# Optimization experiments

Hardware: AMD Instinct MI355X
Metric: run time of the kernel (lower is better)

## Reference

```python
import jax, jax.numpy as jnp
import numpy as np

N_QUBITS = 10
N_GEN = 4
Q_DEPTH = 6
BATCH = 1024


def _cz_chain_diag(n):
    # Diagonal of the CZ chain CZ(0,1) CZ(1,2) ... CZ(n-2,n-1):
    # phase (-1)^(# adjacent 1-1 pairs) per computational basis state.
    idx = np.arange(2 ** n)
    bits = (idx[:, None] >> np.arange(n - 1, -1, -1)) & 1  # wire 0 = most significant (PennyLane)
    pairs = (bits[:, :-1] & bits[:, 1:]).sum(axis=1)
    return ((-1.0) ** pairs).astype(np.float32).reshape((2,) * n)

_CZ = jnp.asarray(_cz_chain_diag(N_QUBITS))


def _ry(t):
    c = jnp.cos(0.5 * t)
    s = jnp.sin(0.5 * t)
    return jnp.stack([jnp.stack([c, -s]), jnp.stack([s, c])]).astype(jnp.complex64)


def _rx(t):
    c = jnp.cos(0.5 * t).astype(jnp.complex64)
    js = (1j * jnp.sin(0.5 * t)).astype(jnp.complex64)
    return jnp.stack([jnp.stack([c, -js]), jnp.stack([-js, c])])


def _apply_1q(state, gate, wire):
    # state: (2,)*n complex statevector; apply 2x2 gate on `wire`.
    state = jnp.moveaxis(state, wire, -1)
    state = jnp.einsum('...j,ij->...i', state, gate)
    return jnp.moveaxis(state, -1, wire)


def _circuit(noise_s, weights, cz):
    # noise_s: (n_qubits,), weights: (q_depth, n_qubits)
    n = noise_s.shape[0]
    state = jnp.zeros((2,) * n, jnp.complex64).at[(0,) * n].set(1.0)
    for q in range(n):
        state = _apply_1q(state, _ry(noise_s[q]), q)
        state = _apply_1q(state, _rx(noise_s[q]), q)

    def layer(st, w):
        for q in range(n):
            st = _apply_1q(st, _ry(w[q]), q)
        return st * cz, None

    state, _ = jax.lax.scan(layer, state, weights)
    # <X_q> = Re <psi| X_q |psi>; X_q flips the q-th wire.
    return jnp.stack([jnp.real(jnp.vdot(state, jnp.flip(state, axis=q))) for q in range(n)])


def setup_inputs() -> dict:
    key = jax.random.key(0)
    k1, k2 = jax.random.split(key)
    noise = jax.random.normal(k1, (BATCH, N_QUBITS), dtype=jnp.float32)
    q_params = jax.random.uniform(k2, (N_GEN, Q_DEPTH, N_QUBITS), dtype=jnp.float32)  # q_delta=1.0 * rand
    return {"noise": noise, "q_params": q_params}


def reference(noise, q_params):
    per_sample = lambda ns, w: _circuit(ns, w, _CZ)
    per_gen = jax.vmap(lambda w: jax.vmap(lambda ns: per_sample(ns, w))(noise))(q_params)  # (G, B, n)
    out = jnp.transpose(per_gen, (1, 0, 2)).reshape(noise.shape[0], N_GEN * N_QUBITS)
    return out.astype(jnp.float32)
```

## Files before the change

### kernel.cpp

```cpp
#include <hip/hip_runtime.h>

#define NQ 10
#define NG 4
#define QD 6
#define NBATCH 1024
#define WPB 4


typedef unsigned u2v __attribute__((ext_vector_type(2)));

template<int CTRL, int RM, int BM, bool BC>
__device__ __forceinline__ float dppmov(float x) {
    return __int_as_float(__builtin_amdgcn_update_dpp(
        0, __float_as_int(x), CTRL, RM, BM, BC));
}
template<int CTRL>
__device__ __forceinline__ float dpp1(float x) { return dppmov<CTRL,0xF,0xF,true>(x); }

struct FX1 { static __device__ __forceinline__ float f(float x){ return dpp1<0xB1>(x); } };
struct FX2 { static __device__ __forceinline__ float f(float x){ return dpp1<0x4E>(x); } };
struct FX4 { static __device__ __forceinline__ float f(float x){ return dpp1<0x1B>(dpp1<0x141>(x)); } };
struct FX8 { static __device__ __forceinline__ float f(float x){ return dpp1<0x128>(x); } };
struct FX16 {
    static __device__ __forceinline__ float f(float x){
        return __int_as_float(__builtin_amdgcn_ds_swizzle(__float_as_int(x), 0x401F));
    }
};
struct FX32 {
    static __device__ __forceinline__ float f(float x){ return __shfl_xor(x, 32, 64); }
};

__device__ __forceinline__ float rlane(float v, int idx) {
    return __int_as_float(__builtin_amdgcn_readlane(__float_as_int(v), idx));
}

#if __has_builtin(__builtin_amdgcn_permlane32_swap) && __has_builtin(__builtin_amdgcn_permlane16_swap)
#define HAVE_SWAP 1
__device__ __forceinline__ void plswap32(float &a, float &b) {
    u2v r = __builtin_amdgcn_permlane32_swap(__float_as_uint(a), __float_as_uint(b), false, false);
    a = __uint_as_float(r.x); b = __uint_as_float(r.y);
}
__device__ __forceinline__ void plswap16(float &a, float &b) {
    u2v r = __builtin_amdgcn_permlane16_swap(__float_as_uint(a), __float_as_uint(b), false, false);
    a = __uint_as_float(r.x); b = __uint_as_float(r.y);
}
__device__ __forceinline__ void tr_b5b3(float (&s)[16]) {
#pragma unroll
    for (int j = 0; j < 8; ++j) plswap32(s[j], s[j + 8]);
}
__device__ __forceinline__ void tr_b4b2(float (&s)[16]) {
#pragma unroll
    for (int jj = 0; jj < 8; ++jj) {
        const int j = (jj & 3) | ((jj >> 2) << 3);
        plswap16(s[j], s[j + 4]);
    }
}
#else
#define HAVE_SWAP 0
#endif

__device__ __forceinline__ float wave_reduce(float x) {
    x += dppmov<0x111,0xF,0xF,true >(x);
    x += dppmov<0x112,0xF,0xF,true >(x);
    x += dppmov<0x114,0xF,0xF,true >(x);
    x += dppmov<0x118,0xF,0xF,true >(x);
    x += dppmov<0x142,0xA,0xF,false>(x);
    x += dppmov<0x143,0xC,0xF,false>(x);
    return __int_as_float(__builtin_amdgcn_readlane(__float_as_int(x), 63));
}

template<int M>
__device__ __forceinline__ void intra_rot1(float (&s)[16], float c, float sn) {
#pragma unroll
    for (int j = 0; j < 16; ++j)
        if ((j & M) == 0) {
            const int k = j | M;
            float v0 = s[j], v1 = s[k];
            s[j] = c * v0 - sn * v1;
            s[k] = sn * v0 + c * v1;
        }
}

template<class PF, int LM>
__device__ __forceinline__ void cross_rot(float (&sr)[16], float (&si)[16],
                                          float c, float sn, int lane) {
    const float sv = (lane & LM) ? sn : -sn;
#pragma unroll
    for (int j = 0; j < 16; ++j) {
        float pr = PF::f(sr[j]);
        sr[j] = c * sr[j] + sv * pr;
        float pi = PF::f(si[j]);
        si[j] = c * si[j] + sv * pi;
    }
}

template<class PF>
__device__ __forceinline__ float cross_exp(const float (&sr)[16], const float (&si)[16]) {
    float a = 0.f;
#pragma unroll
    for (int j = 0; j < 16; ++j) {
        a += sr[j] * PF::f(sr[j]);
        a += si[j] * PF::f(si[j]);
    }
    return a;
}

template<int M>
__device__ __forceinline__ float intra_exp(const float (&sr)[16], const float (&si)[16]) {
    float a = 0.f;
#pragma unroll
    for (int j = 0; j < 16; ++j)
        a += sr[j] * sr[j ^ M] + si[j] * si[j ^ M];
    return a;
}

__global__ __launch_bounds__(64 * WPB) void qsim_kernel(
    const float* __restrict__ noise,
    const float* __restrict__ qp,
    float* __restrict__ out)
{
    const int wave = threadIdx.x >> 6;
    const int lane = threadIdx.x & 63;
    const int g    = blockIdx.x & 3;
    const int b    = (blockIdx.x >> 2) * WPB + wave;

    float wcv, wsv;
    {
        const int widx = (lane < QD * NQ) ? lane : 0;
        __sincosf(0.5f * qp[g * (QD * NQ) + widx], &wsv, &wcv);
    }

    float sr[16], si[16];
    {
        float nc[NQ], ns[NQ];
#pragma unroll
        for (int q = 0; q < NQ; ++q)
            __sincosf(0.5f * noise[b * NQ + q], &ns[q], &nc[q]);

        auto facr = [&](int q, int bit) { return bit ? nc[q]*ns[q] : nc[q]*nc[q]; };
        auto faci = [&](int q, int bit) { return bit ? -nc[q]*ns[q] : -ns[q]*ns[q]; };

        float hr = 1.f, hi = 0.f;
#pragma unroll
        for (int p = 4; p <= 9; ++p) {
            const int q = NQ - 1 - p, bit = (lane >> (p - 4)) & 1;
            float fr = facr(q, bit), fi = faci(q, bit);
            float tr = hr * fr - hi * fi;
            float ti = hr * fi + hi * fr;
            hr = tr; hi = ti;
        }
        float t01r[4], t01i[4], t23r[4], t23i[4];
#pragma unroll
        for (int a = 0; a < 4; ++a) {
            float f9r = facr(9, a & 1), f9i = faci(9, a & 1);
            float f8r = facr(8, (a >> 1) & 1), f8i = faci(8, (a >> 1) & 1);
            t01r[a] = f9r * f8r - f9i * f8i;
            t01i[a] = f9r * f8i + f9i * f8r;
            float f7r = facr(7, a & 1), f7i = faci(7, a & 1);
            float f6r = facr(6, (a >> 1) & 1), f6i = faci(6, (a >> 1) & 1);
            t23r[a] = f7r * f6r - f7i * f6i;
            t23i[a] = f7r * f6i + f7i * f6r;
        }
        float prer[4], prei[4];
#pragma unroll
        for (int a = 0; a < 4; ++a) {
            prer[a] = hr * t01r[a] - hi * t01i[a];
            prei[a] = hr * t01i[a] + hi * t01r[a];
        }
#pragma unroll
        for (int j = 0; j < 16; ++j) {
            sr[j] = prer[j & 3] * t23r[j >> 2] - prei[j & 3] * t23i[j >> 2];
            si[j] = prer[j & 3] * t23i[j >> 2] + prei[j & 3] * t23r[j >> 2];
        }
    }

    unsigned czm[16];
#pragma unroll
    for (int j = 0; j < 16; ++j) {
        unsigned i = ((unsigned)lane << 4) | (unsigned)j;
        czm[j] = (unsigned)(__popc(i & (i >> 1)) & 1) << 31;
    }

#pragma unroll 1
    for (int l = 0; l < QD; ++l) {
        const int base = l * NQ;
        float c[NQ], sn[NQ];
#pragma unroll
        for (int q = 0; q < NQ; ++q) {
            c[q]  = rlane(wcv, base + q);
            sn[q] = rlane(wsv, base + q);
        }

        intra_rot1<1>(sr, c[9], sn[9]); intra_rot1<1>(si, c[9], sn[9]);
        intra_rot1<2>(sr, c[8], sn[8]); intra_rot1<2>(si, c[8], sn[8]);
        intra_rot1<4>(sr, c[7], sn[7]); intra_rot1<4>(si, c[7], sn[7]);
        intra_rot1<8>(sr, c[6], sn[6]); intra_rot1<8>(si, c[6], sn[6]);
        cross_rot<FX1, 1>(sr, si, c[5], sn[5], lane);
        cross_rot<FX2, 2>(sr, si, c[4], sn[4], lane);
        cross_rot<FX4, 4>(sr, si, c[3], sn[3], lane);
        cross_rot<FX8, 8>(sr, si, c[2], sn[2], lane);
#if HAVE_SWAP
        tr_b5b3(sr); tr_b5b3(si);
        tr_b4b2(sr); tr_b4b2(si);
        intra_rot1<8>(sr, c[0], sn[0]); intra_rot1<8>(si, c[0], sn[0]);
        intra_rot1<4>(sr, c[1], sn[1]); intra_rot1<4>(si, c[1], sn[1]);
        tr_b4b2(sr); tr_b4b2(si);
        tr_b5b3(sr); tr_b5b3(si);
#else
        cross_rot<FX32,32>(sr, si, c[0], sn[0], lane);
        cross_rot<FX16,16>(sr, si, c[1], sn[1], lane);
#endif
#pragma unroll
        for (int j = 0; j < 16; ++j) {
            sr[j] = __uint_as_float(__float_as_uint(sr[j]) ^ czm[j]);
            si[j] = __uint_as_float(__float_as_uint(si[j]) ^ czm[j]);
        }
    }

    float outval = 0.f;
    {
        float e9 = wave_reduce(intra_exp<1>(sr, si));
        float e8 = wave_reduce(intra_exp<2>(sr, si));
        float e7 = wave_reduce(intra_exp<4>(sr, si));
        float e6 = wave_reduce(intra_exp<8>(sr, si));
        float e5 = wave_reduce(cross_exp<FX1>(sr, si));
        float e4 = wave_reduce(cross_exp<FX2>(sr, si));
        float e3 = wave_reduce(cross_exp<FX4>(sr, si));
        float e2 = wave_reduce(cross_exp<FX8>(sr, si));
        float e0, e1;
#if HAVE_SWAP
        tr_b5b3(sr); tr_b5b3(si);
        tr_b4b2(sr); tr_b4b2(si);
        e0 = wave_reduce(intra_exp<8>(sr, si));
        e1 = wave_reduce(intra_exp<4>(sr, si));
#else
        e0 = wave_reduce(cross_exp<FX32>(sr, si));
        e1 = wave_reduce(cross_exp<FX16>(sr, si));
#endif
        outval = (lane == 0) ? e0 : outval;
        outval = (lane == 1) ? e1 : outval;
        outval = (lane == 2) ? e2 : outval;
        outval = (lane == 3) ? e3 : outval;
        outval = (lane == 4) ? e4 : outval;
        outval = (lane == 5) ? e5 : outval;
        outval = (lane == 6) ? e6 : outval;
        outval = (lane == 7) ? e7 : outval;
        outval = (lane == 8) ? e8 : outval;
        outval = (lane == 9) ? e9 : outval;
    }

    if (lane < NQ)
        out[b * (NG * NQ) + g * NQ + lane] = outval;
}

extern "C" void kernel_launch(void* const* d_in, const int* in_sizes, int n_in,
                              void* d_out, int out_size, void* d_ws, size_t ws_size,
                              hipStream_t stream) {
    const float* noise = (const float*)d_in[0];
    const float* qp    = (const float*)d_in[1];
    float* out = (float*)d_out;

    const int nblocks = (NBATCH * NG) / WPB;
    qsim_kernel<<<nblocks, 64 * WPB, 0, stream>>>(noise, qp, out);
}
```

Before: 99.51 us.

## Factor cosines out of RY rotations and apply combined scale at output

Each RY rotation is rewritten as [1,-t;t,1] with t=tan(theta/2). This turns every pair update into a single FMA, and the product of all cosines (squared) is applied once to the final expectation values. The CZ sign masks are now derived from four per-lane constants instead of a 16-entry array, which lowers register use, and the launch bounds now ask for 2 blocks per CU. This removes multiplies and half the readlanes per layer, but tan can blow up for angles near pi, and there is a numerical risk if cos is near zero.

```diff
diff --git a/kernel.cpp b/kernel.cpp
--- a/kernel.cpp
+++ b/kernel.cpp
@@ -69,28 +69,36 @@
     return __int_as_float(__builtin_amdgcn_readlane(__float_as_int(x), 63));
 }
 
+__device__ __forceinline__ float wave_product(float x) {
+    x *= dpp1<0xB1>(x);
+    x *= dpp1<0x4E>(x);
+    x *= dpp1<0x1B>(dpp1<0x141>(x));
+    x *= dpp1<0x128>(x);
+    x *= FX16::f(x);
+    x *= FX32::f(x);
+    return x;
+}
+
 template<int M>
-__device__ __forceinline__ void intra_rot1(float (&s)[16], float c, float sn) {
+__device__ __forceinline__ void intra_rot_t(float (&s)[16], float t) {
 #pragma unroll
     for (int j = 0; j < 16; ++j)
         if ((j & M) == 0) {
             const int k = j | M;
             float v0 = s[j], v1 = s[k];
-            s[j] = c * v0 - sn * v1;
-            s[k] = sn * v0 + c * v1;
+            s[j] = fmaf(-t, v1, v0);
+            s[k] = fmaf( t, v0, v1);
         }
 }
 
 template<class PF, int LM>
-__device__ __forceinline__ void cross_rot(float (&sr)[16], float (&si)[16],
-                                          float c, float sn, int lane) {
-    const float sv = (lane & LM) ? sn : -sn;
+__device__ __forceinline__ void cross_rot_t(float (&sr)[16], float (&si)[16],
+                                            float t, int lane) {
+    const float sv = (lane & LM) ? t : -t;
 #pragma unroll
     for (int j = 0; j < 16; ++j) {
-        float pr = PF::f(sr[j]);
-        sr[j] = c * sr[j] + sv * pr;
-        float pi = PF::f(si[j]);
-        si[j] = c * si[j] + sv * pi;
+        sr[j] = fmaf(PF::f(sr[j]), sv, sr[j]);
+        si[j] = fmaf(PF::f(si[j]), sv, si[j]);
     }
 }
 
@@ -99,8 +107,8 @@
     float a = 0.f;
 #pragma unroll
     for (int j = 0; j < 16; ++j) {
-        a += sr[j] * PF::f(sr[j]);
-        a += si[j] * PF::f(si[j]);
+        a = fmaf(PF::f(sr[j]), sr[j], a);
+        a = fmaf(PF::f(si[j]), si[j], a);
     }
     return a;
 }
@@ -114,7 +122,7 @@
     return a;
 }
 
-__global__ __launch_bounds__(64 * WPB) void qsim_kernel(
+__global__ __launch_bounds__(256, 2) void qsim_kernel(
     const float* __restrict__ noise,
     const float* __restrict__ qp,
     float* __restrict__ out)
@@ -124,10 +132,15 @@
     const int g    = blockIdx.x & 3;
     const int b    = (blockIdx.x >> 2) * WPB + wave;
 
-    float wcv, wsv;
+    float wt, scale2;
     {
         const int widx = (lane < QD * NQ) ? lane : 0;
-        __sincosf(0.5f * qp[g * (QD * NQ) + widx], &wsv, &wcv);
+        float sv, cv;
+        __sincosf(0.5f * qp[g * (QD * NQ) + widx], &sv, &cv);
+        wt = sv / cv;
+        float cvc = (lane < QD * NQ) ? cv : 1.0f;
+        float p = wave_product(cvc);
+        scale2 = p * p;
     }
 
     float sr[16], si[16];
@@ -174,46 +187,47 @@
         }
     }
 
-    unsigned czm[16];
-#pragma unroll
-    for (int j = 0; j < 16; ++j) {
-        unsigned i = ((unsigned)lane << 4) | (unsigned)j;
-        czm[j] = (unsigned)(__popc(i & (i >> 1)) & 1) << 31;
+    unsigned mE, mEn, mO, mOn;
+    {
+        unsigned par_l = (unsigned)(__popc(lane & (lane >> 1)) & 1) << 31;
+        mE  = par_l;
+        mEn = mE ^ 0x80000000u;
+        mO  = mE ^ ((unsigned)(lane & 1) << 31);
+        mOn = mO ^ 0x80000000u;
     }
 
 #pragma unroll 1
     for (int l = 0; l < QD; ++l) {
         const int base = l * NQ;
-        float c[NQ], sn[NQ];
-#pragma unroll
-        for (int q = 0; q < NQ; ++q) {
-            c[q]  = rlane(wcv, base + q);
-            sn[q] = rlane(wsv, base + q);
-        }
-
-        intra_rot1<1>(sr, c[9], sn[9]); intra_rot1<1>(si, c[9], sn[9]);
-        intra_rot1<2>(sr, c[8], sn[8]); intra_rot1<2>(si, c[8], sn[8]);
-        intra_rot1<4>(sr, c[7], sn[7]); intra_rot1<4>(si, c[7], sn[7]);
-        intra_rot1<8>(sr, c[6], sn[6]); intra_rot1<8>(si, c[6], sn[6]);
-        cross_rot<FX1, 1>(sr, si, c[5], sn[5], lane);
-        cross_rot<FX2, 2>(sr, si, c[4], sn[4], lane);
-        cross_rot<FX4, 4>(sr, si, c[3], sn[3], lane);
-        cross_rot<FX8, 8>(sr, si, c[2], sn[2], lane);
+        float t[NQ];
+#pragma unroll
+        for (int q = 0; q < NQ; ++q) t[q] = rlane(wt, base + q);
+
+        intra_rot_t<1>(sr, t[9]); intra_rot_t<1>(si, t[9]);
+        intra_rot_t<2>(sr, t[8]); intra_rot_t<2>(si, t[8]);
+        intra_rot_t<4>(sr, t[7]); intra_rot_t<4>(si, t[7]);
+        intra_rot_t<8>(sr, t[6]); intra_rot_t<8>(si, t[6]);
+        cross_rot_t<FX1, 1>(sr, si, t[5], lane);
+        cross_rot_t<FX2, 2>(sr, si, t[4], lane);
+        cross_rot_t<FX4, 4>(sr, si, t[3], lane);
+        cross_rot_t<FX8, 8>(sr, si, t[2], lane);
 #if HAVE_SWAP
         tr_b5b3(sr); tr_b5b3(si);
         tr_b4b2(sr); tr_b4b2(si);
-        intra_rot1<8>(sr, c[0], sn[0]); intra_rot1<8>(si, c[0], sn[0]);
-        intra_rot1<4>(sr, c[1], sn[1]); intra_rot1<4>(si, c[1], sn[1]);
+        intra_rot_t<8>(sr, t[0]); intra_rot_t<8>(si, t[0]);
+        intra_rot_t<4>(sr, t[1]); intra_rot_t<4>(si, t[1]);
         tr_b4b2(sr); tr_b4b2(si);
         tr_b5b3(sr); tr_b5b3(si);
 #else
-        cross_rot<FX32,32>(sr, si, c[0], sn[0], lane);
-        cross_rot<FX16,16>(sr, si, c[1], sn[1], lane);
+        cross_rot_t<FX32,32>(sr, si, t[0], lane);
+        cross_rot_t<FX16,16>(sr, si, t[1], lane);
 #endif
 #pragma unroll
         for (int j = 0; j < 16; ++j) {
-            sr[j] = __uint_as_float(__float_as_uint(sr[j]) ^ czm[j]);
-            si[j] = __uint_as_float(__float_as_uint(si[j]) ^ czm[j]);
+            const bool jpar = (__popc(j & (j >> 1)) & 1) != 0;
+            const unsigned m = (j & 8) ? (jpar ? mOn : mO) : (jpar ? mEn : mE);
+            sr[j] = __uint_as_float(__float_as_uint(sr[j]) ^ m);
+            si[j] = __uint_as_float(__float_as_uint(si[j]) ^ m);
         }
     }
 
@@ -250,7 +264,7 @@
     }
 
     if (lane < NQ)
-        out[b * (NG * NQ) + g * NQ + lane] = outval;
+        out[b * (NG * NQ) + g * NQ + lane] = outval * scale2;
 }
 
 extern "C" void kernel_launch(void* const* d_in, const int* in_sizes, int n_in,
```

Result: faster. 87.61 us (-12.0%).
